# Kernel optimization log

Measured on AMD Instinct MI355X. Metric: run time of the kernel, lower is better.

The kernel has to match this reference:

```python
import jax, jax.numpy as jnp
import numpy as np

SEQ_LEN = 128
INPUT_DIM = 256
HIDDEN_DIM = 1024
NUM_CLASSES = 10
BATCH = 1024


def setup_inputs() -> dict:
    key = jax.random.key(0)
    ks = jax.random.split(key, 12)
    D, H, C = INPUT_DIM, HIDDEN_DIM, NUM_CLASSES
    s = 0.02
    return {
        "x": jax.random.randint(ks[0], (BATCH, SEQ_LEN), 0, SEQ_LEN),
        "embed_w": jax.random.normal(ks[1], (SEQ_LEN, D), dtype=jnp.float32),
        "w_g": jax.random.normal(ks[2], (H, D + H), dtype=jnp.float32) * s,
        "w_i": jax.random.normal(ks[3], (H, D + H), dtype=jnp.float32) * s,
        "w_f": jax.random.normal(ks[4], (H, D + H), dtype=jnp.float32) * s,
        "w_o": jax.random.normal(ks[5], (H, D + H), dtype=jnp.float32) * s,
        "b_g": jax.random.normal(ks[6], (H,), dtype=jnp.float32) * s,
        "b_i": jax.random.normal(ks[7], (H,), dtype=jnp.float32) * s,
        "b_f": jax.random.normal(ks[8], (H,), dtype=jnp.float32) * s,
        "b_o": jax.random.normal(ks[9], (H,), dtype=jnp.float32) * s,
        "w_p": jax.random.normal(ks[10], (C, H), dtype=jnp.float32) * s,
        "b_p": jax.random.normal(ks[11], (C,), dtype=jnp.float32) * s,
    }


def reference(x, embed_w, w_g, w_i, w_f, w_o, b_g, b_i, b_f, b_o, w_p, b_p):
    B = x.shape[0]
    H = w_g.shape[0]
    embeds = embed_w[x]  # [B, S, D]
    h0 = jnp.zeros((B, H), dtype=embed_w.dtype)
    c0 = jnp.zeros((B, H), dtype=embed_w.dtype)

    # Faithful to the original, which calls cell_forward(t, h, c) against a
    # signature (x, c, h) and assigns h, c = (new_c, new_h).
    def step(carry, xt):
        h, c = carry
        x_h = jnp.concatenate([xt, c], axis=1)  # original concats x with its 'h' param == c
        g = jnp.tanh(x_h @ w_g.T + b_g)
        i = jax.nn.sigmoid(x_h @ w_i.T + b_i)
        f = jax.nn.sigmoid(x_h @ w_f.T + b_f)
        o = jax.nn.sigmoid(x_h @ w_o.T + b_o)
        new_c = g * i + h * f  # original's 'c' param == h
        new_h = jnp.tanh(new_c) * o
        return (new_c, new_h), None  # assigned back as h, c = new_c, new_h

    (h, c), _ = jax.lax.scan(step, (h0, c0), jnp.transpose(embeds, (1, 0, 2)))
    return jax.nn.softmax(h @ w_p.T + b_p, axis=1)
```

## Files before the change

### kernel.cpp

```cpp
#include <hip/hip_runtime.h>
#include <hip/hip_bf16.h>


typedef __attribute__((ext_vector_type(8))) short bf16x8;
typedef __attribute__((ext_vector_type(4))) float f32x4;

#define GLOBAL_AS __attribute__((address_space(1)))
#define LDS_AS    __attribute__((address_space(3)))

static __device__ __forceinline__ void async_copy16(const void* g, void* l) {
    __builtin_amdgcn_global_load_lds((const GLOBAL_AS void*)g, (LDS_AS void*)l, 16, 0, 0);
}
static __device__ __forceinline__ float sigm(float x) {
    return 1.f / (1.f + __expf(-x));
}
static __device__ __forceinline__ float tanh_fast(float x) {
    return 1.f - 2.f / (__expf(2.f * x) + 1.f);
}

__global__ __launch_bounds__(256) void prep_table(
    const float* __restrict__ embed,
    const float* __restrict__ wg, const float* __restrict__ wi,
    const float* __restrict__ wf, const float* __restrict__ wo,
    const float* __restrict__ bg, const float* __restrict__ bi,
    const float* __restrict__ bff, const float* __restrict__ bo,
    float* __restrict__ T)
{
    __shared__ float e[8][256];
    const int tid = threadIdx.x;
    const int col = blockIdx.x * 256 + tid;
    const int s0 = blockIdx.y * 8;
    const int j = col >> 2, g = col & 3;
    const float* w = (g == 0 ? wg : g == 1 ? wi : g == 2 ? wf : wo) + (size_t)j * 1280;
    const float bias = (g == 0 ? bg : g == 1 ? bi : g == 2 ? bff : bo)[j];
    #pragma unroll
    for (int i = 0; i < 8; ++i) e[i][tid] = embed[(s0 + i) * 256 + tid];
    __syncthreads();
    const float4* w4 = (const float4*)w;
    float acc[8];
    #pragma unroll
    for (int i = 0; i < 8; ++i) acc[i] = bias;
    for (int d = 0; d < 64; ++d) {
        const float4 wv = w4[d];
        #pragma unroll
        for (int i = 0; i < 8; ++i) {
            const float4 ev = ((const float4*)e[i])[d];
            acc[i] += ev.x * wv.x + ev.y * wv.y + ev.z * wv.z + ev.w * wv.w;
        }
    }
    #pragma unroll
    for (int i = 0; i < 8; ++i)
        T[(size_t)(s0 + i) * 4096 + col] = acc[i];
}

__global__ __launch_bounds__(256) void pack_w(
    const float* __restrict__ wg, const float* __restrict__ wi,
    const float* __restrict__ wf, const float* __restrict__ wo,
    __hip_bfloat16* __restrict__ Wt)
{
    const int col = blockIdx.x;
    const int j = col >> 2, g = col & 3;
    const float* w = (g == 0 ? wg : g == 1 ? wi : g == 2 ? wf : wo)
                     + (size_t)j * 1280 + 256;
    __hip_bfloat16* out = Wt + (size_t)col * 1024;
    for (int k = threadIdx.x; k < 1024; k += 256)
        out[k] = __float2bfloat16(w[k]);
}

__global__ __launch_bounds__(512, 4) void step_fused(
    const __hip_bfloat16* __restrict__ Wt,
    const float* __restrict__ T,
    const int* __restrict__ X,
    const __hip_bfloat16* __restrict__ Hprev,
    __hip_bfloat16* __restrict__ Hnext,
    float* __restrict__ CSblob,
    float* __restrict__ CSout,
    int t)
{
    __shared__ char lds[3][24576];
    const int tid = threadIdx.x;
    const int w = tid >> 6, l = tid & 63;
    const int wm = w >> 1, wn = w & 1;
    const int wcol0 = (blockIdx.x & 31) * 128;
    const int batch0 = (blockIdx.x >> 5) * 64;

#define STAGE(K0, BUF) do {                                                    \
        _Pragma("unroll")                                                      \
        for (int i_ = 0; i_ < 2; ++i_) {                                       \
            const int sW = tid + i_ * 512;                                     \
            const int rW = sW >> 3, cW = sW & 7;                               \
            async_copy16(Wt + (size_t)(wcol0 + rW) * 1024 + (K0)               \
                             + ((cW ^ (rW & 7)) << 3),                         \
                         &lds[BUF][sW * 16]);                                  \
        }                                                                      \
        const int sH = tid;                                                    \
        const int rH = sH >> 3, cH = sH & 7;                                   \
        async_copy16(Hprev + (size_t)(batch0 + rH) * 1024 + (K0)               \
                         + ((cH ^ (rH & 7)) << 3),                             \
                     &lds[BUF][16384 + sH * 16]);                              \
    } while (0)

    STAGE(0, 0);
    STAGE(64, 1);

    int batchN[2], jM[2];
    #pragma unroll
    for (int n = 0; n < 2; ++n) batchN[n] = batch0 + wn * 32 + n * 16 + (l & 15);
    #pragma unroll
    for (int m = 0; m < 2; ++m) jM[m] = (wcol0 >> 2) + wm * 8 + m * 4 + (l >> 4);

    f32x4 tv[2][2];
    float ap[2][2];
    #pragma unroll
    for (int n = 0; n < 2; ++n) {
        const int s = X[batchN[n] * 128 + t];
        #pragma unroll
        for (int m = 0; m < 2; ++m)
            tv[m][n] = *(const f32x4*)&T[(size_t)s * 4096 + jM[m] * 4];
    }
    float* blob = CSblob + ((size_t)blockIdx.x * 512 + tid) * 4;
    if (t > 0) {
        #pragma unroll
        for (int m = 0; m < 2; ++m)
            #pragma unroll
            for (int n = 0; n < 2; ++n) ap[m][n] = blob[m * 2 + n];
    } else {
        #pragma unroll
        for (int m = 0; m < 2; ++m)
            #pragma unroll
            for (int n = 0; n < 2; ++n) ap[m][n] = 0.f;
    }

    f32x4 acc[2][2];
    const f32x4 z4 = {0.f, 0.f, 0.f, 0.f};
    #pragma unroll
    for (int m = 0; m < 2; ++m)
        #pragma unroll
        for (int n = 0; n < 2; ++n) acc[m][n] = z4;

    #pragma unroll
    for (int kt = 0; kt < 16; ++kt) {
        if (kt == 15) asm volatile("s_waitcnt vmcnt(0)" ::: "memory");
        else          asm volatile("s_waitcnt vmcnt(3)" ::: "memory");
        __builtin_amdgcn_s_barrier();
        if (kt < 14) STAGE((kt + 2) * 64, (kt + 2) % 3);

        const char* base = &lds[kt % 3][0];
        bf16x8 af0[2], bfr0[2], af1[2], bfr1[2];
        #pragma unroll
        for (int m = 0; m < 2; ++m) {
            const int row = wm * 32 + m * 16 + (l & 15);
            const int ch0 = (l >> 4) ^ (row & 7);
            const int ch1 = (4 + (l >> 4)) ^ (row & 7);
            af0[m] = *(const bf16x8*)(base + (row * 8 + ch0) * 16);
            af1[m] = *(const bf16x8*)(base + (row * 8 + ch1) * 16);
        }
        #pragma unroll
        for (int n = 0; n < 2; ++n) {
            const int row = wn * 32 + n * 16 + (l & 15);
            const int ch0 = (l >> 4) ^ (row & 7);
            const int ch1 = (4 + (l >> 4)) ^ (row & 7);
            bfr0[n] = *(const bf16x8*)(base + 16384 + (row * 8 + ch0) * 16);
            bfr1[n] = *(const bf16x8*)(base + 16384 + (row * 8 + ch1) * 16);
        }
        __builtin_amdgcn_s_setprio(1);
        #pragma unroll
        for (int m = 0; m < 2; ++m)
            #pragma unroll
            for (int n = 0; n < 2; ++n)
                acc[m][n] = __builtin_amdgcn_mfma_f32_16x16x32_bf16(
                    af0[m], bfr0[n], acc[m][n], 0, 0, 0);
        #pragma unroll
        for (int m = 0; m < 2; ++m)
            #pragma unroll
            for (int n = 0; n < 2; ++n)
                acc[m][n] = __builtin_amdgcn_mfma_f32_16x16x32_bf16(
                    af1[m], bfr1[n], acc[m][n], 0, 0, 0);
        __builtin_amdgcn_s_setprio(0);
    }
#undef STAGE

    #pragma unroll
    for (int m = 0; m < 2; ++m)
        #pragma unroll
        for (int n = 0; n < 2; ++n) {
            const float z0 = acc[m][n][0] + tv[m][n][0];
            const float z1 = acc[m][n][1] + tv[m][n][1];
            const float z2 = acc[m][n][2] + tv[m][n][2];
            const float z3 = acc[m][n][3] + tv[m][n][3];
            const float gg = tanh_fast(z0);
            const float ii = sigm(z1);
            const float ff = sigm(z2);
            const float oo = sigm(z3);
            const float na = gg * ii + ap[m][n] * ff;
            blob[m * 2 + n] = na;
            Hnext[(size_t)batchN[n] * 1024 + jM[m]] =
                __float2bfloat16(tanh_fast(na) * oo);
            if (t == 127)
                CSout[(size_t)batchN[n] * 1024 + jM[m]] = na;
        }
}

__global__ __launch_bounds__(256) void proj_softmax(
    const float* __restrict__ A,
    const float* __restrict__ Wp,
    const float* __restrict__ bp,
    float* __restrict__ out)
{
    const int row = blockIdx.x;
    const float* a = A + (size_t)row * 1024;
    float p[10];
    #pragma unroll
    for (int c = 0; c < 10; ++c) p[c] = 0.f;
    for (int k = threadIdx.x; k < 1024; k += 256) {
        const float av = a[k];
        #pragma unroll
        for (int c = 0; c < 10; ++c) p[c] += av * Wp[c * 1024 + k];
    }
    #pragma unroll
    for (int c = 0; c < 10; ++c)
        #pragma unroll
        for (int off = 32; off; off >>= 1) p[c] += __shfl_down(p[c], off);
    __shared__ float red[4][10];
    const int wv = threadIdx.x >> 6, ln = threadIdx.x & 63;
    if (ln == 0)
        for (int c = 0; c < 10; ++c) red[wv][c] = p[c];
    __syncthreads();
    if (threadIdx.x == 0) {
        float logits[10], mx = -1e30f;
        for (int c = 0; c < 10; ++c) {
            logits[c] = red[0][c] + red[1][c] + red[2][c] + red[3][c] + bp[c];
            mx = fmaxf(mx, logits[c]);
        }
        float sum = 0.f;
        for (int c = 0; c < 10; ++c) { logits[c] = __expf(logits[c] - mx); sum += logits[c]; }
        const float inv = 1.f / sum;
        for (int c = 0; c < 10; ++c) out[(size_t)row * 10 + c] = logits[c] * inv;
    }
}

extern "C" void kernel_launch(void* const* d_in, const int* in_sizes, int n_in,
                              void* d_out, int out_size, void* d_ws, size_t ws_size,
                              hipStream_t stream) {
    (void)in_sizes; (void)n_in; (void)out_size; (void)ws_size;
    const int*   x     = (const int*)d_in[0];
    const float* embed = (const float*)d_in[1];
    const float* wg    = (const float*)d_in[2];
    const float* wi    = (const float*)d_in[3];
    const float* wf    = (const float*)d_in[4];
    const float* wo    = (const float*)d_in[5];
    const float* bg    = (const float*)d_in[6];
    const float* bi    = (const float*)d_in[7];
    const float* bff   = (const float*)d_in[8];
    const float* bo    = (const float*)d_in[9];
    const float* wp    = (const float*)d_in[10];
    const float* bp    = (const float*)d_in[11];
    float* out = (float*)d_out;

    char* ws = (char*)d_ws;
    float*          T    = (float*)(ws);
    __hip_bfloat16* Wt   = (__hip_bfloat16*)(ws + (2u << 20));
    __hip_bfloat16* BhA  = (__hip_bfloat16*)(ws + (10u << 20));
    __hip_bfloat16* BhB  = (__hip_bfloat16*)(ws + (12u << 20));
    float*          CSo  = (float*)(ws + (14u << 20));
    float*          CSb  = (float*)(ws + (18u << 20));

    prep_table<<<dim3(16, 16), 256, 0, stream>>>(embed, wg, wi, wf, wo, bg, bi, bff, bo, T);
    pack_w<<<4096, 256, 0, stream>>>(wg, wi, wf, wo, Wt);
    hipMemsetAsync(BhA, 0, (size_t)1024 * 1024 * sizeof(__hip_bfloat16), stream);

    for (int t = 0; t < 128; ++t) {
        const __hip_bfloat16* Hp = (t & 1) ? BhB : BhA;
        __hip_bfloat16*       Hn = (t & 1) ? BhA : BhB;
        step_fused<<<512, 512, 0, stream>>>(Wt, T, x, Hp, Hn, CSb, CSo, t);
    }
    proj_softmax<<<1024, 256, 0, stream>>>(CSo, wp, bp, out);
}
```

Measured before the change: 2.158 ms.

## Replace per-timestep launches with persistent cooperative kernel using grid sync

Swaps the 128 per-step kernel launches for one cooperative persistent kernel of 256 blocks that loops over timesteps and calls grid.sync() between them. The cell state stays in registers instead of going through a global blob, and the next step's table rows are prefetched before the gate math. Each block's tile grows to 128 batch rows with a K-step of 32. The goal is to remove launch overhead and the cell-state round trips through memory, at the cost of grid-wide barrier latency, lower occupancy and reliance on all blocks being co-resident.

```diff
diff --git a/kernel.cpp b/kernel.cpp
--- a/kernel.cpp
+++ b/kernel.cpp
@@ -1,5 +1,8 @@
 #include <hip/hip_runtime.h>
 #include <hip/hip_bf16.h>
+#include <hip/hip_cooperative_groups.h>
+
+namespace cg = cooperative_groups;
 
 
 typedef __attribute__((ext_vector_type(8))) short bf16x8;
@@ -67,138 +70,142 @@
         out[k] = __float2bfloat16(w[k]);
 }
 
-__global__ __launch_bounds__(512, 4) void step_fused(
+__global__ __launch_bounds__(512, 2) void lstm_persist(
     const __hip_bfloat16* __restrict__ Wt,
     const float* __restrict__ T,
     const int* __restrict__ X,
-    const __hip_bfloat16* __restrict__ Hprev,
-    __hip_bfloat16* __restrict__ Hnext,
-    float* __restrict__ CSblob,
-    float* __restrict__ CSout,
-    int t)
-{
-    __shared__ char lds[3][24576];
+    __hip_bfloat16* __restrict__ BhA,
+    __hip_bfloat16* __restrict__ BhB,
+    float* __restrict__ CSout)
+{
+    __shared__ char lds[3][16384];
     const int tid = threadIdx.x;
     const int w = tid >> 6, l = tid & 63;
     const int wm = w >> 1, wn = w & 1;
     const int wcol0 = (blockIdx.x & 31) * 128;
-    const int batch0 = (blockIdx.x >> 5) * 64;
-
-#define STAGE(K0, BUF) do {                                                    \
-        _Pragma("unroll")                                                      \
-        for (int i_ = 0; i_ < 2; ++i_) {                                       \
-            const int sW = tid + i_ * 512;                                     \
-            const int rW = sW >> 3, cW = sW & 7;                               \
-            async_copy16(Wt + (size_t)(wcol0 + rW) * 1024 + (K0)               \
-                             + ((cW ^ (rW & 7)) << 3),                         \
-                         &lds[BUF][sW * 16]);                                  \
-        }                                                                      \
-        const int sH = tid;                                                    \
-        const int rH = sH >> 3, cH = sH & 7;                                   \
-        async_copy16(Hprev + (size_t)(batch0 + rH) * 1024 + (K0)               \
-                         + ((cH ^ (rH & 7)) << 3),                             \
-                     &lds[BUF][16384 + sH * 16]);                              \
-    } while (0)
-
-    STAGE(0, 0);
-    STAGE(64, 1);
-
-    int batchN[2], jM[2];
-    #pragma unroll
-    for (int n = 0; n < 2; ++n) batchN[n] = batch0 + wn * 32 + n * 16 + (l & 15);
+    const int batch0 = (blockIdx.x >> 5) * 128;
+
+    cg::grid_group grid = cg::this_grid();
+
+    int batchN[4], jM[2];
+    #pragma unroll
+    for (int n = 0; n < 4; ++n) batchN[n] = batch0 + wn * 64 + n * 16 + (l & 15);
     #pragma unroll
     for (int m = 0; m < 2; ++m) jM[m] = (wcol0 >> 2) + wm * 8 + m * 4 + (l >> 4);
 
-    f32x4 tv[2][2];
-    float ap[2][2];
-    #pragma unroll
-    for (int n = 0; n < 2; ++n) {
-        const int s = X[batchN[n] * 128 + t];
+    float cs[2][4];
+    #pragma unroll
+    for (int m = 0; m < 2; ++m)
+        #pragma unroll
+        for (int n = 0; n < 4; ++n) cs[m][n] = 0.f;
+
+    f32x4 tv[2][4];
+    #pragma unroll
+    for (int n = 0; n < 4; ++n) {
+        const int s = X[batchN[n] * 128 + 0];
         #pragma unroll
         for (int m = 0; m < 2; ++m)
             tv[m][n] = *(const f32x4*)&T[(size_t)s * 4096 + jM[m] * 4];
     }
-    float* blob = CSblob + ((size_t)blockIdx.x * 512 + tid) * 4;
-    if (t > 0) {
+
+#define STAGE(K0, BUF) do {                                                    \
+        const int r_ = tid >> 2, c_ = tid & 3;                                 \
+        const int kq_ = (K0) + ((c_ ^ (r_ & 3)) << 3);                         \
+        async_copy16(Wt + (size_t)(wcol0 + r_) * 1024 + kq_,                   \
+                     &lds[BUF][tid * 16]);                                     \
+        async_copy16(Hp + (size_t)(batch0 + r_) * 1024 + kq_,                  \
+                     &lds[BUF][8192 + tid * 16]);                              \
+    } while (0)
+
+    for (int t = 0; t < 128; ++t) {
+        const __hip_bfloat16* Hp = (t & 1) ? BhB : BhA;
+        __hip_bfloat16*       Hn = (t & 1) ? BhA : BhB;
+
+        STAGE(0, 0);
+        STAGE(32, 1);
+
+        f32x4 acc[2][4];
+        const f32x4 z4 = {0.f, 0.f, 0.f, 0.f};
         #pragma unroll
         for (int m = 0; m < 2; ++m)
             #pragma unroll
-            for (int n = 0; n < 2; ++n) ap[m][n] = blob[m * 2 + n];
-    } else {
+            for (int n = 0; n < 4; ++n) acc[m][n] = z4;
+
+        #pragma unroll
+        for (int kt = 0; kt < 32; ++kt) {
+            if (kt == 31) asm volatile("s_waitcnt vmcnt(0)" ::: "memory");
+            else          asm volatile("s_waitcnt vmcnt(2)" ::: "memory");
+            __builtin_amdgcn_s_barrier();
+            if (kt < 30) STAGE((kt + 2) * 32, (kt + 2) % 3);
+
+            const char* base = &lds[kt % 3][0];
+            bf16x8 af[2], bfr[4];
+            #pragma unroll
+            for (int m = 0; m < 2; ++m) {
+                const int row = wm * 32 + m * 16 + (l & 15);
+                const int ch = (l >> 4) ^ (row & 3);
+                af[m] = *(const bf16x8*)(base + (row * 4 + ch) * 16);
+            }
+            #pragma unroll
+            for (int n = 0; n < 4; ++n) {
+                const int row = wn * 64 + n * 16 + (l & 15);
+                const int ch = (l >> 4) ^ (row & 3);
+                bfr[n] = *(const bf16x8*)(base + 8192 + (row * 4 + ch) * 16);
+            }
+            __builtin_amdgcn_s_setprio(1);
+            #pragma unroll
+            for (int m = 0; m < 2; ++m)
+                #pragma unroll
+                for (int n = 0; n < 4; ++n)
+                    acc[m][n] = __builtin_amdgcn_mfma_f32_16x16x32_bf16(
+                        af[m], bfr[n], acc[m][n], 0, 0, 0);
+            __builtin_amdgcn_s_setprio(0);
+        }
+
+        f32x4 tvn[2][4];
+        if (t < 127) {
+            #pragma unroll
+            for (int n = 0; n < 4; ++n) {
+                const int s = X[batchN[n] * 128 + t + 1];
+                #pragma unroll
+                for (int m = 0; m < 2; ++m)
+                    tvn[m][n] = *(const f32x4*)&T[(size_t)s * 4096 + jM[m] * 4];
+            }
+        }
+
         #pragma unroll
         for (int m = 0; m < 2; ++m)
             #pragma unroll
-            for (int n = 0; n < 2; ++n) ap[m][n] = 0.f;
-    }
-
-    f32x4 acc[2][2];
-    const f32x4 z4 = {0.f, 0.f, 0.f, 0.f};
+            for (int n = 0; n < 4; ++n) {
+                const float z0 = acc[m][n][0] + tv[m][n][0];
+                const float z1 = acc[m][n][1] + tv[m][n][1];
+                const float z2 = acc[m][n][2] + tv[m][n][2];
+                const float z3 = acc[m][n][3] + tv[m][n][3];
+                const float gg = tanh_fast(z0);
+                const float ii = sigm(z1);
+                const float ff = sigm(z2);
+                const float oo = sigm(z3);
+                const float na = gg * ii + cs[m][n] * ff;
+                cs[m][n] = na;
+                Hn[(size_t)batchN[n] * 1024 + jM[m]] =
+                    __float2bfloat16(tanh_fast(na) * oo);
+            }
+        if (t < 127) {
+            #pragma unroll
+            for (int m = 0; m < 2; ++m)
+                #pragma unroll
+                for (int n = 0; n < 4; ++n) tv[m][n] = tvn[m][n];
+        }
+
+        if (t < 127) grid.sync();
+    }
+#undef STAGE
+
     #pragma unroll
     for (int m = 0; m < 2; ++m)
         #pragma unroll
-        for (int n = 0; n < 2; ++n) acc[m][n] = z4;
-
-    #pragma unroll
-    for (int kt = 0; kt < 16; ++kt) {
-        if (kt == 15) asm volatile("s_waitcnt vmcnt(0)" ::: "memory");
-        else          asm volatile("s_waitcnt vmcnt(3)" ::: "memory");
-        __builtin_amdgcn_s_barrier();
-        if (kt < 14) STAGE((kt + 2) * 64, (kt + 2) % 3);
-
-        const char* base = &lds[kt % 3][0];
-        bf16x8 af0[2], bfr0[2], af1[2], bfr1[2];
-        #pragma unroll
-        for (int m = 0; m < 2; ++m) {
-            const int row = wm * 32 + m * 16 + (l & 15);
-            const int ch0 = (l >> 4) ^ (row & 7);
-            const int ch1 = (4 + (l >> 4)) ^ (row & 7);
-            af0[m] = *(const bf16x8*)(base + (row * 8 + ch0) * 16);
-            af1[m] = *(const bf16x8*)(base + (row * 8 + ch1) * 16);
-        }
-        #pragma unroll
-        for (int n = 0; n < 2; ++n) {
-            const int row = wn * 32 + n * 16 + (l & 15);
-            const int ch0 = (l >> 4) ^ (row & 7);
-            const int ch1 = (4 + (l >> 4)) ^ (row & 7);
-            bfr0[n] = *(const bf16x8*)(base + 16384 + (row * 8 + ch0) * 16);
-            bfr1[n] = *(const bf16x8*)(base + 16384 + (row * 8 + ch1) * 16);
-        }
-        __builtin_amdgcn_s_setprio(1);
-        #pragma unroll
-        for (int m = 0; m < 2; ++m)
-            #pragma unroll
-            for (int n = 0; n < 2; ++n)
-                acc[m][n] = __builtin_amdgcn_mfma_f32_16x16x32_bf16(
-                    af0[m], bfr0[n], acc[m][n], 0, 0, 0);
-        #pragma unroll
-        for (int m = 0; m < 2; ++m)
-            #pragma unroll
-            for (int n = 0; n < 2; ++n)
-                acc[m][n] = __builtin_amdgcn_mfma_f32_16x16x32_bf16(
-                    af1[m], bfr1[n], acc[m][n], 0, 0, 0);
-        __builtin_amdgcn_s_setprio(0);
-    }
-#undef STAGE
-
-    #pragma unroll
-    for (int m = 0; m < 2; ++m)
-        #pragma unroll
-        for (int n = 0; n < 2; ++n) {
-            const float z0 = acc[m][n][0] + tv[m][n][0];
-            const float z1 = acc[m][n][1] + tv[m][n][1];
-            const float z2 = acc[m][n][2] + tv[m][n][2];
-            const float z3 = acc[m][n][3] + tv[m][n][3];
-            const float gg = tanh_fast(z0);
-            const float ii = sigm(z1);
-            const float ff = sigm(z2);
-            const float oo = sigm(z3);
-            const float na = gg * ii + ap[m][n] * ff;
-            blob[m * 2 + n] = na;
-            Hnext[(size_t)batchN[n] * 1024 + jM[m]] =
-                __float2bfloat16(tanh_fast(na) * oo);
-            if (t == 127)
-                CSout[(size_t)batchN[n] * 1024 + jM[m]] = na;
-        }
+        for (int n = 0; n < 4; ++n)
+            CSout[(size_t)batchN[n] * 1024 + jM[m]] = cs[m][n];
 }
 
 __global__ __launch_bounds__(256) void proj_softmax(
@@ -263,16 +270,14 @@
     __hip_bfloat16* BhA  = (__hip_bfloat16*)(ws + (10u << 20));
     __hip_bfloat16* BhB  = (__hip_bfloat16*)(ws + (12u << 20));
     float*          CSo  = (float*)(ws + (14u << 20));
-    float*          CSb  = (float*)(ws + (18u << 20));
 
     prep_table<<<dim3(16, 16), 256, 0, stream>>>(embed, wg, wi, wf, wo, bg, bi, bff, bo, T);
     pack_w<<<4096, 256, 0, stream>>>(wg, wi, wf, wo, Wt);
     hipMemsetAsync(BhA, 0, (size_t)1024 * 1024 * sizeof(__hip_bfloat16), stream);
 
-    for (int t = 0; t < 128; ++t) {
-        const __hip_bfloat16* Hp = (t & 1) ? BhB : BhA;
-        __hip_bfloat16*       Hn = (t & 1) ? BhA : BhB;
-        step_fused<<<512, 512, 0, stream>>>(Wt, T, x, Hp, Hn, CSb, CSo, t);
-    }
+    void* args[] = {(void*)&Wt, (void*)&T, (void*)&x, (void*)&BhA, (void*)&BhB,
+                    (void*)&CSo};
+    hipLaunchCooperativeKernel((void*)lstm_persist, dim3(256), dim3(512), args, 0, stream);
+
     proj_softmax<<<1024, 256, 0, stream>>>(CSo, wp, bp, out);
 }
```

Result: slower. 5.550 ms (+157.2%).
